# Performance work log

Hardware: AMD Instinct MI355X
Metric: run time of the kernel (lower is better)

Reference implementation:

```python
import jax, jax.numpy as jnp
import numpy as np


def _trilinear(vol, coords, limit):
    """Trilinear interpolation. vol: (C,L,L,L); coords: (H,W,3) in (x,y,z) order
    where x indexes the last vol axis, y the second-to-last, z the third-to-last.
    Returns (C,H,W). Coordinates are clamped to the valid range (SliceExtractor
    with limit=D)."""
    c = jnp.clip(coords, 0.0, limit - 1.0)
    x, y, z = c[..., 0], c[..., 1], c[..., 2]
    x0 = jnp.floor(x); y0 = jnp.floor(y); z0 = jnp.floor(z)
    fx = x - x0; fy = y - y0; fz = z - z0
    x0i = x0.astype(jnp.int32); y0i = y0.astype(jnp.int32); z0i = z0.astype(jnp.int32)
    x1i = jnp.minimum(x0i + 1, limit - 1)
    y1i = jnp.minimum(y0i + 1, limit - 1)
    z1i = jnp.minimum(z0i + 1, limit - 1)

    def g(zi, yi, xi):
        return vol[:, zi, yi, xi]  # (C,H,W) advanced-index gather

    return (g(z0i, y0i, x0i) * ((1 - fz) * (1 - fy) * (1 - fx))
            + g(z0i, y0i, x1i) * ((1 - fz) * (1 - fy) * fx)
            + g(z0i, y1i, x0i) * ((1 - fz) * fy * (1 - fx))
            + g(z0i, y1i, x1i) * ((1 - fz) * fy * fx)
            + g(z1i, y0i, x0i) * (fz * (1 - fy) * (1 - fx))
            + g(z1i, y0i, x1i) * (fz * (1 - fy) * fx)
            + g(z1i, y1i, x0i) * (fz * fy * (1 - fx))
            + g(z1i, y1i, x1i) * (fz * fy * fx))


def setup_inputs() -> dict:
    key = jax.random.key(0)
    k1, k2, k3 = jax.random.split(key, 3)
    B, D = 8, 256
    protein_samples = jax.random.normal(k1, (B, 2, D, D, D), dtype=jnp.float32)
    rotation_samples = jax.random.normal(k2, (B, 3, 3), dtype=jnp.float32)
    translation_samples = jax.random.uniform(k3, (B, 2), dtype=jnp.float32)
    return {"protein_samples": protein_samples,
            "rotation_samples": rotation_samples,
            "translation_samples": translation_samples}


def reference(protein_samples, rotation_samples, translation_samples):
    B = protein_samples.shape[0]
    D = protein_samples.shape[-1]
    Df = jnp.float32(D)

    # base central slice: (D,D,3) coords (x, y, 0) centered at the origin
    coords1d = jnp.arange(D, dtype=jnp.float32) - Df / 2.0
    gy, gx = jnp.meshgrid(coords1d, coords1d, indexing='ij')
    base = jnp.stack([gx, gy, jnp.zeros_like(gx)], axis=-1)  # (D,D,3)

    # rotate slice coords: row-vector coords @ R^T  (bmm(base, R.permute(0,2,1)))
    Rt = jnp.transpose(rotation_samples, (0, 2, 1))  # (B,3,3)
    sl = jnp.einsum('hwc,bcd->bhwd', base, Rt) + Df / 2.0  # (B,D,D,3), shifted to [0,D)

    # Fourier-slice extraction: trilinear gather from the 3D volume
    proj = jax.vmap(_trilinear, in_axes=(0, 0, None))(protein_samples, sl, D)  # (B,2,D,D)
    proj = jnp.transpose(proj, (0, 1, 3, 2)) * jnp.sqrt(Df)

    # translation -> phase shift in Fourier space
    t = -translation_samples.reshape(B, 2)
    t = jnp.stack([t[:, 1], t[:, 0]], axis=1) * (Df / 2.0)  # pixel shifts, swapped
    k = jnp.arange(D, dtype=jnp.float32) - (D // 2)  # centered frequencies
    ang = (-2.0 * jnp.pi / Df) * (t[:, 0][:, None, None] * k[None, :, None]
                                  + t[:, 1][:, None, None] * k[None, None, :])  # (B,D,D)
    cs, sn = jnp.cos(ang), jnp.sin(ang)
    re, im = proj[:, 0], proj[:, 1]
    # complex multiply (re + i*im) * exp(i*ang)
    return jnp.stack([re * cs - im * sn, re * sn + im * cs], axis=1)  # (B,2,D,D)
```

## Files before the change

kernel.cpp:

```cpp
#include <hip/hip_runtime.h>
#include <math.h>

#define DD 256
#define DHALF 128.0f

__global__ __launch_bounds__(256) void slice_extract_phase_kernel(
    const float* __restrict__ vol,
    const float* __restrict__ rot,
    const float* __restrict__ trans,
    float* __restrict__ out)
{
    const int tid = blockIdx.x * blockDim.x + threadIdx.x;
    const int j = tid & (DD - 1);
    const int i = (tid >> 8) & (DD - 1);
    const int b = tid >> 16;

    const float r00 = rot[b * 9 + 0];
    const float r01 = rot[b * 9 + 1];
    const float r10 = rot[b * 9 + 3];
    const float r11 = rot[b * 9 + 4];
    const float r20 = rot[b * 9 + 6];
    const float r21 = rot[b * 9 + 7];

    const float px = (float)i - DHALF;
    const float py = (float)j - DHALF;

    float x = fmaf(r00, px, fmaf(r01, py, DHALF));
    float y = fmaf(r10, px, fmaf(r11, py, DHALF));
    float z = fmaf(r20, px, fmaf(r21, py, DHALF));

    x = fminf(fmaxf(x, 0.0f), 255.0f);
    y = fminf(fmaxf(y, 0.0f), 255.0f);
    z = fminf(fmaxf(z, 0.0f), 255.0f);

    const float x0f = floorf(x), y0f = floorf(y), z0f = floorf(z);
    const float fx = x - x0f, fy = y - y0f, fz = z - z0f;
    const int x0 = (int)x0f, y0 = (int)y0f, z0 = (int)z0f;
    const int x1 = min(x0 + 1, DD - 1);
    const int y1 = min(y0 + 1, DD - 1);
    const int z1 = min(z0 + 1, DD - 1);

    const float gx0 = 1.0f - fx, gy0 = 1.0f - fy, gz0 = 1.0f - fz;
    const float w000 = gz0 * gy0 * gx0;
    const float w001 = gz0 * gy0 * fx;
    const float w010 = gz0 * fy * gx0;
    const float w011 = gz0 * fy * fx;
    const float w100 = fz * gy0 * gx0;
    const float w101 = fz * gy0 * fx;
    const float w110 = fz * fy * gx0;
    const float w111 = fz * fy * fx;

    const size_t plane = (size_t)DD * DD;
    const size_t cstride = plane * DD;
    const float* v0 = vol + (size_t)b * 2 * cstride;
    const float* v1 = v0 + cstride;

    const size_t z0o = (size_t)z0 * plane, z1o = (size_t)z1 * plane;
    const size_t y0o = (size_t)y0 * DD, y1o = (size_t)y1 * DD;

    const size_t o00 = z0o + y0o;
    const size_t o01 = z0o + y1o;
    const size_t o10 = z1o + y0o;
    const size_t o11 = z1o + y1o;

    float re =
        v0[o00 + x0] * w000 + v0[o00 + x1] * w001 +
        v0[o01 + x0] * w010 + v0[o01 + x1] * w011 +
        v0[o10 + x0] * w100 + v0[o10 + x1] * w101 +
        v0[o11 + x0] * w110 + v0[o11 + x1] * w111;
    float im =
        v1[o00 + x0] * w000 + v1[o00 + x1] * w001 +
        v1[o01 + x0] * w010 + v1[o01 + x1] * w011 +
        v1[o10 + x0] * w100 + v1[o10 + x1] * w101 +
        v1[o11 + x0] * w110 + v1[o11 + x1] * w111;

    re *= 16.0f;
    im *= 16.0f;

    const float t0 = -trans[b * 2 + 1] * DHALF;
    const float t1 = -trans[b * 2 + 0] * DHALF;
    const float ki = (float)i - DHALF;
    const float kj = (float)j - DHALF;
    const float ang = (-2.0f * (float)M_PI / 256.0f) * (t0 * ki + t1 * kj);

    float sn, cs;
    sincosf(ang, &sn, &cs);

    const size_t ob = (size_t)b * 2 * plane + (size_t)i * DD + j;
    out[ob]         = re * cs - im * sn;
    out[ob + plane] = re * sn + im * cs;
}

extern "C" void kernel_launch(void* const* d_in, const int* in_sizes, int n_in,
                              void* d_out, int out_size, void* d_ws, size_t ws_size,
                              hipStream_t stream) {
    const float* vol   = (const float*)d_in[0];
    const float* rot   = (const float*)d_in[1];
    const float* trans = (const float*)d_in[2];
    float* out = (float*)d_out;

    const int B = in_sizes[0] / (2 * DD * DD * DD);
    const int total = B * DD * DD;
    dim3 block(256);
    dim3 grid(total / 256);
    slice_extract_phase_kernel<<<grid, block, 0, stream>>>(vol, rot, trans, out);
}
```

Measured before the change: 1.150 ms.

## Tile output into 16x16 blocks interleaved across batches, hoist gathers, use hardware sin/cos

Each block now covers a 16x16 output tile instead of one output row. Block indices interleave the batch index in the low bits, so neighbouring blocks sample different volumes and the gathers of a 2D tile touch a more compact region of the volume, giving better cache locality. All 16 voxel loads are issued before the weight arithmetic to raise memory-level parallelism. sincosf is replaced with range reduction to revolutions plus the amdgcn sin/cos builtins, which are cheaper but less precise. Batch count is hardcoded to 8 through the `& 7` index mask.

```diff
diff --git a/kernel.cpp b/kernel.cpp
--- a/kernel.cpp
+++ b/kernel.cpp
@@ -3,6 +3,7 @@
 
 #define DD 256
 #define DHALF 128.0f
+#define TILE 16
 
 __global__ __launch_bounds__(256) void slice_extract_phase_kernel(
     const float* __restrict__ vol,
@@ -10,10 +11,12 @@
     const float* __restrict__ trans,
     float* __restrict__ out)
 {
-    const int tid = blockIdx.x * blockDim.x + threadIdx.x;
-    const int j = tid & (DD - 1);
-    const int i = (tid >> 8) & (DD - 1);
-    const int b = tid >> 16;
+    const int b    = blockIdx.x & 7;
+    const int tile = blockIdx.x >> 3;
+    const int ti   = tile >> 4;
+    const int tj   = tile & 15;
+    const int i = ti * TILE + (threadIdx.x >> 4);
+    const int j = tj * TILE + (threadIdx.x & 15);
 
     const float r00 = rot[b * 9 + 0];
     const float r01 = rot[b * 9 + 1];
@@ -40,6 +43,27 @@
     const int y1 = min(y0 + 1, DD - 1);
     const int z1 = min(z0 + 1, DD - 1);
 
+    const size_t plane = (size_t)DD * DD;
+    const size_t cstride = plane * DD;
+    const float* v0 = vol + (size_t)b * 2 * cstride;
+    const float* v1 = v0 + cstride;
+
+    const size_t z0o = (size_t)z0 * plane, z1o = (size_t)z1 * plane;
+    const size_t y0o = (size_t)y0 * DD,    y1o = (size_t)y1 * DD;
+    const size_t o00 = z0o + y0o;
+    const size_t o01 = z0o + y1o;
+    const size_t o10 = z1o + y0o;
+    const size_t o11 = z1o + y1o;
+
+    const float a000 = v0[o00 + x0], a001 = v0[o00 + x1];
+    const float a010 = v0[o01 + x0], a011 = v0[o01 + x1];
+    const float a100 = v0[o10 + x0], a101 = v0[o10 + x1];
+    const float a110 = v0[o11 + x0], a111 = v0[o11 + x1];
+    const float b000 = v1[o00 + x0], b001 = v1[o00 + x1];
+    const float b010 = v1[o01 + x0], b011 = v1[o01 + x1];
+    const float b100 = v1[o10 + x0], b101 = v1[o10 + x1];
+    const float b110 = v1[o11 + x0], b111 = v1[o11 + x1];
+
     const float gx0 = 1.0f - fx, gy0 = 1.0f - fy, gz0 = 1.0f - fz;
     const float w000 = gz0 * gy0 * gx0;
     const float w001 = gz0 * gy0 * fx;
@@ -50,41 +74,21 @@
     const float w110 = fz * fy * gx0;
     const float w111 = fz * fy * fx;
 
-    const size_t plane = (size_t)DD * DD;
-    const size_t cstride = plane * DD;
-    const float* v0 = vol + (size_t)b * 2 * cstride;
-    const float* v1 = v0 + cstride;
-
-    const size_t z0o = (size_t)z0 * plane, z1o = (size_t)z1 * plane;
-    const size_t y0o = (size_t)y0 * DD, y1o = (size_t)y1 * DD;
-
-    const size_t o00 = z0o + y0o;
-    const size_t o01 = z0o + y1o;
-    const size_t o10 = z1o + y0o;
-    const size_t o11 = z1o + y1o;
-
-    float re =
-        v0[o00 + x0] * w000 + v0[o00 + x1] * w001 +
-        v0[o01 + x0] * w010 + v0[o01 + x1] * w011 +
-        v0[o10 + x0] * w100 + v0[o10 + x1] * w101 +
-        v0[o11 + x0] * w110 + v0[o11 + x1] * w111;
-    float im =
-        v1[o00 + x0] * w000 + v1[o00 + x1] * w001 +
-        v1[o01 + x0] * w010 + v1[o01 + x1] * w011 +
-        v1[o10 + x0] * w100 + v1[o10 + x1] * w101 +
-        v1[o11 + x0] * w110 + v1[o11 + x1] * w111;
+    float re = a000 * w000 + a001 * w001 + a010 * w010 + a011 * w011 +
+               a100 * w100 + a101 * w101 + a110 * w110 + a111 * w111;
+    float im = b000 * w000 + b001 * w001 + b010 * w010 + b011 * w011 +
+               b100 * w100 + b101 * w101 + b110 * w110 + b111 * w111;
 
     re *= 16.0f;
     im *= 16.0f;
 
     const float t0 = -trans[b * 2 + 1] * DHALF;
     const float t1 = -trans[b * 2 + 0] * DHALF;
-    const float ki = (float)i - DHALF;
-    const float kj = (float)j - DHALF;
-    const float ang = (-2.0f * (float)M_PI / 256.0f) * (t0 * ki + t1 * kj);
-
-    float sn, cs;
-    sincosf(ang, &sn, &cs);
+    const float S  = fmaf(t0, px, t1 * py);
+    const float rev = S * (1.0f / 256.0f);
+    const float m  = rev - rintf(rev);
+    const float sn = __builtin_amdgcn_sinf(-m);
+    const float cs = __builtin_amdgcn_cosf(m);
 
     const size_t ob = (size_t)b * 2 * plane + (size_t)i * DD + j;
     out[ob]         = re * cs - im * sn;
@@ -100,8 +104,8 @@
     float* out = (float*)d_out;
 
     const int B = in_sizes[0] / (2 * DD * DD * DD);
-    const int total = B * DD * DD;
+    const int tiles = (DD / TILE) * (DD / TILE);
     dim3 block(256);
-    dim3 grid(total / 256);
+    dim3 grid(tiles * B);
     slice_extract_phase_kernel<<<grid, block, 0, stream>>>(vol, rot, trans, out);
 }
```

Result: no change. 1.154 ms (+0.4%).
